# Optimization experiments

Measured on AMD Instinct MI355X. Metric: run time of the kernel, lower is better.

The kernel has to match this reference:

```python
import jax, jax.numpy as jnp
import numpy as np

N_NODES = 50000
IN_CH = 128
OUT_CH = 64
N_EDGES = 800000


def setup_inputs() -> dict:
    key = jax.random.key(0)
    k1, k2, k3, k4 = jax.random.split(key, 4)
    z = jax.random.normal(k1, (N_NODES, IN_CH), dtype=jnp.float32)
    edge_index = jax.random.randint(k2, (2, N_EDGES), 0, N_NODES, dtype=jnp.int64)
    # GCNConv params: weight [in, out] (glorot-ish), bias [out]
    W = jax.random.normal(k3, (IN_CH, OUT_CH), dtype=jnp.float32) / np.sqrt(IN_CH)
    b = jnp.zeros((OUT_CH,), dtype=jnp.float32)
    return {"z": z, "edge_index": edge_index, "W": W, "b": b}


def reference(z, edge_index, W, b):
    N = z.shape[0]
    # linear transform first (out_channels < in_channels reduces message traffic)
    x = z @ W  # [N, out]
    # add self-loops
    loop = jnp.arange(N, dtype=edge_index.dtype)
    src = jnp.concatenate([edge_index[0], loop])
    dst = jnp.concatenate([edge_index[1], loop])
    # symmetric normalization deg^-1/2 (degree counted on dst, incl. self-loops)
    deg = jnp.zeros((N,), dtype=x.dtype).at[dst].add(1.0)
    dinv = jnp.where(deg > 0, jax.lax.rsqrt(deg), 0.0)
    norm = dinv[src] * dinv[dst]  # [E+N]
    msg = x[src] * norm[:, None]  # gather + scale
    out = jax.ops.segment_sum(msg, dst, num_segments=N)  # scatter-add
    return jax.nn.relu(out + b)
```

## Files before the change

### kernel.cpp

```cpp
#include <hip/hip_runtime.h>

#define IN_CH 128
#define OUT_CH 64

#define CSHIFT 6
#define BNODES 64
#define NCMAX 1024
#define CAP 1536
#define BIN_EPT 8

typedef __attribute__((ext_vector_type(8))) short bf16x8;
typedef __attribute__((ext_vector_type(4))) float f32x4;

__device__ inline unsigned short f2bf(float x) {
    unsigned int u = __builtin_bit_cast(unsigned int, x);
    return (unsigned short)((u + 0x7FFFu + ((u >> 16) & 1u)) >> 16);
}
__device__ inline float bf2f(unsigned short h) {
    unsigned int u = ((unsigned int)h) << 16;
    return __builtin_bit_cast(float, u);
}

__global__ void bin_edges(const int* __restrict__ ei, int* __restrict__ gctr,
                          unsigned int* __restrict__ ebuf, int E, int NC) {
    __shared__ int cnt[NCMAX];
    __shared__ int gbase[NCMAX];
    for (int i = threadIdx.x; i < NC; i += blockDim.x) cnt[i] = 0;
    __syncthreads();

    unsigned int pk[BIN_EPT];
    int bk[BIN_EPT];
    const int g0 = (blockIdx.x * blockDim.x + threadIdx.x) * BIN_EPT;

    if (g0 + BIN_EPT <= E) {
        int4 s0 = *(const int4*)(ei + g0);
        int4 s1 = *(const int4*)(ei + g0 + 4);
        int4 d0 = *(const int4*)(ei + E + g0);
        int4 d1 = *(const int4*)(ei + E + g0 + 4);
        int ss[BIN_EPT] = {s0.x, s0.y, s0.z, s0.w, s1.x, s1.y, s1.z, s1.w};
        int dd[BIN_EPT] = {d0.x, d0.y, d0.z, d0.w, d1.x, d1.y, d1.z, d1.w};
#pragma unroll
        for (int k = 0; k < BIN_EPT; ++k) {
            pk[k] = ((unsigned int)dd[k] << 16) | (unsigned int)ss[k];
            bk[k] = dd[k] >> CSHIFT;
            atomicAdd(&cnt[bk[k]], 1);
        }
    } else {
#pragma unroll
        for (int k = 0; k < BIN_EPT; ++k) {
            int e = g0 + k;
            if (e < E) {
                int s = ei[e];
                int d = ei[E + e];
                pk[k] = ((unsigned int)d << 16) | (unsigned int)s;
                bk[k] = d >> CSHIFT;
                atomicAdd(&cnt[bk[k]], 1);
            } else bk[k] = -1;
        }
    }
    __syncthreads();
    for (int i = threadIdx.x; i < NC; i += blockDim.x) {
        int c = cnt[i];
        gbase[i] = c ? atomicAdd(&gctr[i], c) : 0;
    }
    __syncthreads();
    for (int i = threadIdx.x; i < NC; i += blockDim.x) cnt[i] = 0;
    __syncthreads();
#pragma unroll
    for (int k = 0; k < BIN_EPT; ++k) {
        if (bk[k] >= 0) {
            int o = gbase[bk[k]] + atomicAdd(&cnt[bk[k]], 1);
            if (o < CAP)
                ebuf[(size_t)bk[k] * CAP + o] = pk[k];
        }
    }
}

__global__ void degree_wfrag(const unsigned int* __restrict__ ebuf,
                             const int* __restrict__ gctr,
                             float* __restrict__ dinv, int N, int NC,
                             const float* __restrict__ W,
                             unsigned short* __restrict__ wf) {
    const int b = blockIdx.x;
    if (b == NC) {
        for (int i = threadIdx.x; i < 4 * 4 * 64 * 8; i += blockDim.x) {
            int j    = i & 7;
            int lane = (i >> 3) & 63;
            int kk   = (i >> 9) & 3;
            int nt   = i >> 11;
            int k = kk * 32 + ((lane >> 4) & 3) * 8 + j;
            int n = nt * 16 + (lane & 15);
            wf[i] = f2bf(W[k * OUT_CH + n]);
        }
        return;
    }
    __shared__ int cnt[BNODES];
    const int n0 = b << CSHIFT;
    if (threadIdx.x < BNODES) cnt[threadIdx.x] = 0;
    __syncthreads();
    const int ecnt = min(gctr[b], CAP);
    const unsigned int* eb = ebuf + (size_t)b * CAP;
    for (int i = threadIdx.x; i < ecnt; i += blockDim.x)
        atomicAdd(&cnt[(int)(eb[i] >> 16) - n0], 1);
    __syncthreads();
    const int node = n0 + threadIdx.x;
    if (threadIdx.x < BNODES && node < N)
        dinv[node] = rsqrtf((float)(cnt[threadIdx.x] + 1));
}

__global__ void gemm_mfma(const float* __restrict__ z,
                          const unsigned short* __restrict__ wfrag,
                          const float* __restrict__ dinv,
                          unsigned short* __restrict__ y, int N) {
    const int lane = threadIdx.x & 63;
    const int wid  = threadIdx.x >> 6;
    const int row0 = blockIdx.x * 64 + wid * 16;

    bf16x8 bfr[4][4];
#pragma unroll
    for (int nt = 0; nt < 4; ++nt)
#pragma unroll
        for (int kk = 0; kk < 4; ++kk)
            bfr[nt][kk] = *(const bf16x8*)&wfrag[(((nt * 4 + kk) * 64) + lane) * 8];

    f32x4 acc[4];
#pragma unroll
    for (int nt = 0; nt < 4; ++nt) acc[nt] = (f32x4){0.f, 0.f, 0.f, 0.f};

    const int arow = row0 + (lane & 15);
    const int zrow = (arow < N) ? arow : (N - 1);
    const int sub  = lane >> 4;
    const float* zr = z + (size_t)zrow * IN_CH + sub * 8;

#pragma unroll
    for (int kk = 0; kk < 4; ++kk) {
        float4 f0 = *(const float4*)(zr + kk * 32);
        float4 f1 = *(const float4*)(zr + kk * 32 + 4);
        bf16x8 a;
        a[0] = (short)f2bf(f0.x); a[1] = (short)f2bf(f0.y);
        a[2] = (short)f2bf(f0.z); a[3] = (short)f2bf(f0.w);
        a[4] = (short)f2bf(f1.x); a[5] = (short)f2bf(f1.y);
        a[6] = (short)f2bf(f1.z); a[7] = (short)f2bf(f1.w);
#pragma unroll
        for (int nt = 0; nt < 4; ++nt)
            acc[nt] = __builtin_amdgcn_mfma_f32_16x16x32_bf16(a, bfr[nt][kk], acc[nt], 0, 0, 0);
    }

    const int crow0 = row0 + sub * 4;
#pragma unroll
    for (int r = 0; r < 4; ++r) {
        int row = crow0 + r;
        if (row < N) {
            float di = dinv[row];
#pragma unroll
            for (int nt = 0; nt < 4; ++nt)
                y[(size_t)row * OUT_CH + nt * 16 + (lane & 15)] = f2bf(acc[nt][r] * di);
        }
    }
}

__global__ __launch_bounds__(512) void sort_gather(const unsigned int* __restrict__ ebuf,
                                                   const int* __restrict__ gctr,
                                                   const unsigned int* __restrict__ y2,
                                                   const float* __restrict__ dinv,
                                                   const float* __restrict__ bias,
                                                   float* __restrict__ out, int N) {
    __shared__ unsigned int epk[CAP];
    __shared__ unsigned short scol[CAP];
    __shared__ int cnt[BNODES];
    __shared__ int off[BNODES];
    const int b = blockIdx.x;
    const int n0 = b << CSHIFT;
    const int tid = threadIdx.x;
    const int ecnt = min(gctr[b], CAP);
    const unsigned int* eb = ebuf + (size_t)b * CAP;

    if (tid < BNODES) cnt[tid] = 0;
    __syncthreads();
    for (int i = tid; i < ecnt; i += 512) {
        unsigned int p = eb[i];
        epk[i] = p;
        atomicAdd(&cnt[(int)(p >> 16) - n0], 1);
    }
    __syncthreads();

    if (tid < BNODES) off[tid] = cnt[tid];
    __syncthreads();
    for (int o = 1; o < BNODES; o <<= 1) {
        int v = 0;
        if (tid < BNODES && tid >= o) v = off[tid - o];
        __syncthreads();
        if (tid < BNODES) off[tid] += v;
        __syncthreads();
    }
    if (tid < BNODES) { off[tid] -= cnt[tid]; cnt[tid] = off[tid]; }
    __syncthreads();

    for (int i = tid; i < ecnt; i += 512) {
        unsigned int p = epk[i];
        int rel = (int)(p >> 16) - n0;
        int slot = atomicAdd(&cnt[rel], 1);
        scol[slot] = (unsigned short)(p & 0xFFFFu);
    }
    __syncthreads();

    const int lane = tid & 63;
    const int w = tid >> 6;
    const int half = lane >> 5;
    const int c2 = lane & 31;
    const float2 bv = *(const float2*)&bias[c2 * 2];

#pragma unroll
    for (int rnd = 0; rnd < 4; ++rnd) {
        const int nrel = rnd * 16 + w * 2 + half;
        const int node = n0 + nrel;
        const bool valid = node < N;
        int jbeg = valid ? off[nrel] : 0;
        int cend = valid ? cnt[nrel] : 0;

        float accLo = 0.f, accHi = 0.f;
        if (valid) {
            unsigned int sv = y2[(size_t)node * 32 + c2];
            accLo = bf2f((unsigned short)(sv & 0xFFFFu));
            accHi = bf2f((unsigned short)(sv >> 16));
        }

        for (int j = jbeg; j < cend; j += 8) {
            unsigned int v[8]; bool m[8];
#pragma unroll
            for (int t = 0; t < 8; ++t) {
                int jj = j + t;
                m[t] = jj < cend;
                int s = scol[m[t] ? jj : (cend - 1)];
                v[t] = y2[(size_t)s * 32 + c2];
            }
#pragma unroll
            for (int t = 0; t < 8; ++t) {
                if (m[t]) {
                    accLo += bf2f((unsigned short)(v[t] & 0xFFFFu));
                    accHi += bf2f((unsigned short)(v[t] >> 16));
                }
            }
        }

        if (valid) {
            float di = dinv[node];
            float2 o2;
            o2.x = fmaxf(fmaf(accLo, di, bv.x), 0.f);
            o2.y = fmaxf(fmaf(accHi, di, bv.y), 0.f);
            *(float2*)&out[(size_t)node * OUT_CH + c2 * 2] = o2;
        }
    }
}

extern "C" void kernel_launch(void* const* d_in, const int* in_sizes, int n_in,
                              void* d_out, int out_size, void* d_ws, size_t ws_size,
                              hipStream_t stream) {
    const float* z  = (const float*)d_in[0];
    const int*   ei = (const int*)d_in[1];
    const float* W  = (const float*)d_in[2];
    const float* b  = (const float*)d_in[3];
    float*       out = (float*)d_out;

    const int N = in_sizes[0] / IN_CH;
    const int E = in_sizes[1] / 2;
    const int NC = (N + BNODES - 1) >> CSHIFT;

    unsigned short* y     = (unsigned short*)d_ws;
    unsigned int*   ebuf  = (unsigned int*)(y + (size_t)N * OUT_CH);
    float*          dinv  = (float*)(ebuf + (size_t)NC * CAP);
    int*            gctr  = (int*)(dinv + N);
    unsigned short* wfrag = (unsigned short*)(((uintptr_t)(gctr + NC) + 15) & ~(uintptr_t)15);

    hipMemsetAsync(gctr, 0, (size_t)NC * sizeof(int), stream);

    const int binBlocks = (E + 256 * BIN_EPT - 1) / (256 * BIN_EPT);

    bin_edges   <<<binBlocks, 256, 0, stream>>>(ei, gctr, ebuf, E, NC);
    degree_wfrag<<<NC + 1, 256, 0, stream>>>(ebuf, gctr, dinv, N, NC, W, wfrag);
    gemm_mfma   <<<(N + 63) / 64, 256, 0, stream>>>(z, wfrag, dinv, y, N);
    sort_gather <<<NC, 512, 0, stream>>>(ebuf, gctr, (const unsigned int*)y, dinv, b, out, N);
}
```

Measured before the change: 72.09 us.

## Precompute per-bucket prefix offsets in degree kernel; remap gather lanes to 16-wide quarter-wave rows

The degree kernel now also computes the exclusive prefix sum of per-node counts and writes it to a new global boff array. The gather kernel then skips its own count pass, scan and staging buffer and builds the sorted column list in one pass. The gather inner loop also changes from 32 lanes per node covering 64 channels to 16 lanes per node with two passes over the channel halves, so each wave serves four nodes. This trades some redundant scan work and an extra global array for fewer barriers and less LDS use, but each edge's row is now gathered with 64-byte segments issued twice.

```diff
diff --git a/kernel.cpp b/kernel.cpp
--- a/kernel.cpp
+++ b/kernel.cpp
@@ -78,7 +78,8 @@
 
 __global__ void degree_wfrag(const unsigned int* __restrict__ ebuf,
                              const int* __restrict__ gctr,
-                             float* __restrict__ dinv, int N, int NC,
+                             float* __restrict__ dinv, int* __restrict__ boff,
+                             int N, int NC,
                              const float* __restrict__ W,
                              unsigned short* __restrict__ wf) {
     const int b = blockIdx.x;
@@ -95,17 +96,30 @@
         return;
     }
     __shared__ int cnt[BNODES];
+    __shared__ int off[BNODES];
+    const int tid = threadIdx.x;
     const int n0 = b << CSHIFT;
-    if (threadIdx.x < BNODES) cnt[threadIdx.x] = 0;
+    if (tid < BNODES) cnt[tid] = 0;
     __syncthreads();
     const int ecnt = min(gctr[b], CAP);
     const unsigned int* eb = ebuf + (size_t)b * CAP;
-    for (int i = threadIdx.x; i < ecnt; i += blockDim.x)
+    for (int i = tid; i < ecnt; i += blockDim.x)
         atomicAdd(&cnt[(int)(eb[i] >> 16) - n0], 1);
     __syncthreads();
-    const int node = n0 + threadIdx.x;
-    if (threadIdx.x < BNODES && node < N)
-        dinv[node] = rsqrtf((float)(cnt[threadIdx.x] + 1));
+    if (tid < BNODES) off[tid] = cnt[tid];
+    __syncthreads();
+    for (int o = 1; o < BNODES; o <<= 1) {
+        int v = 0;
+        if (tid < BNODES && tid >= o) v = off[tid - o];
+        __syncthreads();
+        if (tid < BNODES) off[tid] += v;
+        __syncthreads();
+    }
+    if (tid < BNODES) {
+        boff[b * BNODES + tid] = off[tid] - cnt[tid];
+        const int node = n0 + tid;
+        if (node < N) dinv[node] = rsqrtf((float)(cnt[tid] + 1));
+    }
 }
 
 __global__ void gemm_mfma(const float* __restrict__ z,
@@ -161,94 +175,85 @@
 
 __global__ __launch_bounds__(512) void sort_gather(const unsigned int* __restrict__ ebuf,
                                                    const int* __restrict__ gctr,
-                                                   const unsigned int* __restrict__ y2,
+                                                   const int* __restrict__ boff,
+                                                   const unsigned int* __restrict__ y32,
                                                    const float* __restrict__ dinv,
                                                    const float* __restrict__ bias,
                                                    float* __restrict__ out, int N) {
-    __shared__ unsigned int epk[CAP];
     __shared__ unsigned short scol[CAP];
-    __shared__ int cnt[BNODES];
-    __shared__ int off[BNODES];
+    __shared__ int off_s[BNODES];
+    __shared__ int cur[BNODES];
     const int b = blockIdx.x;
     const int n0 = b << CSHIFT;
     const int tid = threadIdx.x;
     const int ecnt = min(gctr[b], CAP);
     const unsigned int* eb = ebuf + (size_t)b * CAP;
 
-    if (tid < BNODES) cnt[tid] = 0;
-    __syncthreads();
+    if (tid < BNODES) {
+        int o = boff[b * BNODES + tid];
+        off_s[tid] = o;
+        cur[tid] = o;
+    }
+    __syncthreads();
+
     for (int i = tid; i < ecnt; i += 512) {
         unsigned int p = eb[i];
-        epk[i] = p;
-        atomicAdd(&cnt[(int)(p >> 16) - n0], 1);
-    }
-    __syncthreads();
-
-    if (tid < BNODES) off[tid] = cnt[tid];
-    __syncthreads();
-    for (int o = 1; o < BNODES; o <<= 1) {
-        int v = 0;
-        if (tid < BNODES && tid >= o) v = off[tid - o];
-        __syncthreads();
-        if (tid < BNODES) off[tid] += v;
-        __syncthreads();
-    }
-    if (tid < BNODES) { off[tid] -= cnt[tid]; cnt[tid] = off[tid]; }
-    __syncthreads();
-
-    for (int i = tid; i < ecnt; i += 512) {
-        unsigned int p = epk[i];
         int rel = (int)(p >> 16) - n0;
-        int slot = atomicAdd(&cnt[rel], 1);
+        int slot = atomicAdd(&cur[rel], 1);
         scol[slot] = (unsigned short)(p & 0xFFFFu);
     }
     __syncthreads();
 
     const int lane = tid & 63;
     const int w = tid >> 6;
-    const int half = lane >> 5;
-    const int c2 = lane & 31;
-    const float2 bv = *(const float2*)&bias[c2 * 2];
-
-#pragma unroll
-    for (int rnd = 0; rnd < 4; ++rnd) {
-        const int nrel = rnd * 16 + w * 2 + half;
+    const int q = lane >> 4;
+    const int c4 = lane & 15;
+
+#pragma unroll
+    for (int rnd = 0; rnd < 2; ++rnd) {
+        const int nrel = rnd * 32 + w * 4 + q;
         const int node = n0 + nrel;
         const bool valid = node < N;
-        int jbeg = valid ? off[nrel] : 0;
-        int cend = valid ? cnt[nrel] : 0;
-
-        float accLo = 0.f, accHi = 0.f;
-        if (valid) {
-            unsigned int sv = y2[(size_t)node * 32 + c2];
-            accLo = bf2f((unsigned short)(sv & 0xFFFFu));
-            accHi = bf2f((unsigned short)(sv >> 16));
-        }
-
-        for (int j = jbeg; j < cend; j += 8) {
-            unsigned int v[8]; bool m[8];
-#pragma unroll
-            for (int t = 0; t < 8; ++t) {
-                int jj = j + t;
-                m[t] = jj < cend;
-                int s = scol[m[t] ? jj : (cend - 1)];
-                v[t] = y2[(size_t)s * 32 + c2];
+        const int jbeg = off_s[nrel];
+        const int jend = (nrel < BNODES - 1) ? off_s[nrel + 1] : ecnt;
+        const float di = valid ? dinv[node] : 0.f;
+
+#pragma unroll
+        for (int pass = 0; pass < 2; ++pass) {
+            const size_t hbase = (size_t)pass * 16 + c4;
+            float accLo = 0.f, accHi = 0.f;
+            if (valid) {
+                unsigned int sv = y32[(size_t)node * 32 + hbase];
+                accLo = bf2f((unsigned short)(sv & 0xFFFFu));
+                accHi = bf2f((unsigned short)(sv >> 16));
             }
-#pragma unroll
-            for (int t = 0; t < 8; ++t) {
-                if (m[t]) {
-                    accLo += bf2f((unsigned short)(v[t] & 0xFFFFu));
-                    accHi += bf2f((unsigned short)(v[t] >> 16));
+
+            for (int j = jbeg; j < jend; j += 8) {
+                unsigned int v[8]; bool m[8];
+#pragma unroll
+                for (int t = 0; t < 8; ++t) {
+                    int jj = j + t;
+                    m[t] = jj < jend;
+                    int s = scol[m[t] ? jj : (jend - 1)];
+                    v[t] = y32[(size_t)s * 32 + hbase];
+                }
+#pragma unroll
+                for (int t = 0; t < 8; ++t) {
+                    if (m[t]) {
+                        accLo += bf2f((unsigned short)(v[t] & 0xFFFFu));
+                        accHi += bf2f((unsigned short)(v[t] >> 16));
+                    }
                 }
             }
-        }
-
-        if (valid) {
-            float di = dinv[node];
-            float2 o2;
-            o2.x = fmaxf(fmaf(accLo, di, bv.x), 0.f);
-            o2.y = fmaxf(fmaf(accHi, di, bv.y), 0.f);
-            *(float2*)&out[(size_t)node * OUT_CH + c2 * 2] = o2;
+
+            if (valid) {
+                const int ch = pass * 32 + c4 * 2;
+                float2 bv = *(const float2*)&bias[ch];
+                float2 o2;
+                o2.x = fmaxf(fmaf(accLo, di, bv.x), 0.f);
+                o2.y = fmaxf(fmaf(accHi, di, bv.y), 0.f);
+                *(float2*)&out[(size_t)node * OUT_CH + ch] = o2;
+            }
         }
     }
 }
@@ -269,7 +274,8 @@
     unsigned short* y     = (unsigned short*)d_ws;
     unsigned int*   ebuf  = (unsigned int*)(y + (size_t)N * OUT_CH);
     float*          dinv  = (float*)(ebuf + (size_t)NC * CAP);
-    int*            gctr  = (int*)(dinv + N);
+    int*            boff  = (int*)(dinv + N);
+    int*            gctr  = boff + (size_t)NC * BNODES;
     unsigned short* wfrag = (unsigned short*)(((uintptr_t)(gctr + NC) + 15) & ~(uintptr_t)15);
 
     hipMemsetAsync(gctr, 0, (size_t)NC * sizeof(int), stream);
@@ -277,7 +283,8 @@
     const int binBlocks = (E + 256 * BIN_EPT - 1) / (256 * BIN_EPT);
 
     bin_edges   <<<binBlocks, 256, 0, stream>>>(ei, gctr, ebuf, E, NC);
-    degree_wfrag<<<NC + 1, 256, 0, stream>>>(ebuf, gctr, dinv, N, NC, W, wfrag);
+    degree_wfrag<<<NC + 1, 256, 0, stream>>>(ebuf, gctr, dinv, boff, N, NC, W, wfrag);
     gemm_mfma   <<<(N + 63) / 64, 256, 0, stream>>>(z, wfrag, dinv, y, N);
-    sort_gather <<<NC, 512, 0, stream>>>(ebuf, gctr, (const unsigned int*)y, dinv, b, out, N);
-}
+    sort_gather <<<NC, 512, 0, stream>>>(ebuf, gctr, boff, (const unsigned int*)y,
+                                         dinv, b, out, N);
+}
```

Result: no change. 72.85 us (+1.1%).
